# Performance work log

Measured on AMD Instinct MI355X. Metric: run time of the kernel, lower is better.

## Reference

```python
import jax, jax.numpy as jnp
import numpy as np

W = 128
POS_FREQ = 10  # -> 3*10*2 = 60 encoded dims
VIEW_FREQ = 4  # -> 3*4*2 = 24 encoded dims


def freq_encode(v, n_freq):
    # tcnn 'Frequency' encoding: sin/cos of 2^j * pi * x per input dim.
    scales = (2.0 ** jnp.arange(n_freq, dtype=v.dtype)) * jnp.pi  # [F]
    ang = v[..., :, None] * scales  # [N, 3, F]
    enc = jnp.stack([jnp.sin(ang), jnp.cos(ang)], axis=-1)  # [N, 3, F, 2]
    return enc.reshape(v.shape[0], -1)  # [N, 3*F*2]


def mlp(h, weights):
    # tcnn FullyFusedMLP: bias-free, ReLU on hidden layers, linear output.
    for Wm in weights[:-1]:
        h = jax.nn.relu(h @ Wm)
    return h @ weights[-1]


def setup_inputs():
    key = jax.random.key(0)
    ks = jax.random.split(key, 10)
    N = 1048576

    def w(k, fan_in, fan_out):
        s = (1.0 / np.sqrt(fan_in)).astype(np.float32)
        return jax.random.uniform(k, (fan_in, fan_out), jnp.float32, -s, s)

    return {
        "x": jax.random.uniform(ks[0], (N, 6), jnp.float32),
        "Wd1_0": w(ks[1], 60, W),
        "Wd1_1": w(ks[2], W, W),
        "Wd1_2": w(ks[3], W, W),
        "Wd2_0": w(ks[4], 60 + W, W),
        "Wd2_1": w(ks[5], W, W),
        "Wd2_2": w(ks[6], W, W),
        "Wd2_3": w(ks[7], W, W + 1),
        "Wc_0": w(ks[8], 24 + W, W),
        "Wc_1": w(ks[9], W, 3),
    }


def reference(x, Wd1_0, Wd1_1, Wd1_2, Wd2_0, Wd2_1, Wd2_2, Wd2_3, Wc_0, Wc_1):
    pos, view = x[:, :3], x[:, 3:6]
    # Density MLP
    enc_pos = freq_encode(pos, POS_FREQ)                # [N, 60]
    part1 = mlp(enc_pos, [Wd1_0, Wd1_1, Wd1_2])          # [N, 128]
    dens_out = mlp(jnp.concatenate([enc_pos, part1], -1),
                   [Wd2_0, Wd2_1, Wd2_2, Wd2_3])         # [N, 129]
    blending = jax.nn.sigmoid(dens_out[:, :1])           # [N, 1]
    feature = dens_out[:, 1:]                            # [N, 128]
    density = feature[:, 0:1]                            # [N, 1]
    # Color MLP
    enc_view = freq_encode(view, VIEW_FREQ)              # [N, 24]
    rgb = mlp(jnp.concatenate([enc_view, feature], -1), [Wc_0, Wc_1])  # [N, 3]
    return jnp.concatenate([rgb, density, blending], -1)  # [N, 5]
```

## Files before the change

kernel.cpp:

```cpp
#include <hip/hip_runtime.h>
#include <cstdint>
#include <cstddef>

typedef __attribute__((ext_vector_type(8))) __bf16 bf16x8;
typedef __attribute__((ext_vector_type(16))) float floatx16;

struct SrcPtrs { const float* p[9]; };


__global__ void prep_zero(unsigned short* __restrict__ ws) {
  uint4* p = (uint4*)ws;
  const int n = 143360 / 8;
  for (int i = blockIdx.x * blockDim.x + threadIdx.x; i < n; i += gridDim.x * blockDim.x)
    p[i] = make_uint4(0u, 0u, 0u, 0u);
}

__global__ void prep_fill(SrcPtrs sp, unsigned short* __restrict__ ws) {
  const int m  = blockIdx.x >> 4;
  const int sl = blockIdx.x & 15;
  const int K[9]  = {60, 128, 128, 188, 128, 128, 128, 152, 128};
  const int N[9]  = {128, 128, 128, 128, 128, 128, 129, 128, 3};
  const int SS[9] = {4, 8, 8, 12, 8, 8, 8, 10, 8};
  const unsigned OFF[9] = {0u, 8192u, 24576u, 40960u, 65536u, 81920u, 98304u, 118784u, 139264u};
  const int Km = K[m], Nm = N[m], Sm = SS[m];
  const float* __restrict__ src = sp.p[m];
  unsigned short* __restrict__ dst = ws + OFF[m];
  const int tot = Km * Nm;
  for (int i = sl * 256 + (int)threadIdx.x; i < tot; i += 16 * 256) {
    int k = i / Nm;
    int n = i - k * Nm;
    int kk = k, row = n;
    if (m == 3) kk = (k < 60) ? 128 + k : k - 60;
    if (m == 7) kk = (k < 24) ? 128 + k : k - 24;
    if (m == 6) row = (n == 0) ? 128 : n - 1;
    const int t = row >> 5, l31 = row & 31;
    const int s = kk >> 4, q2 = (kk >> 3) & 1, j = kk & 7;
    dst[(t * Sm + s) * 512 + (q2 * 32 + l31) * 8 + j] =
        __builtin_bit_cast(unsigned short, (__bf16)src[i]);
  }
}


#if defined(__has_builtin)
#if __has_builtin(__builtin_amdgcn_permlane32_swap)
#define HAVE_PLSWAP 1
#endif
#endif
#ifndef HAVE_PLSWAP
#define HAVE_PLSWAP 0
#endif

__device__ __forceinline__ unsigned pk2(float a, float b) {
  unsigned short ua = __builtin_bit_cast(unsigned short, (__bf16)a);
  unsigned short ub = __builtin_bit_cast(unsigned short, (__bf16)b);
  return (unsigned)ua | ((unsigned)ub << 16);
}

__device__ __forceinline__ void stage16(const void* g, void* l) {
  __builtin_amdgcn_global_load_lds(
      (const __attribute__((address_space(1))) unsigned int*)g,
      (__attribute__((address_space(3))) unsigned int*)l, 16, 0, 0);
}

__device__ __forceinline__ void half_swap(unsigned a, unsigned b, int q2,
                                          unsigned& lo, unsigned& hi) {
#if HAVE_PLSWAP
  auto r = __builtin_amdgcn_permlane32_swap(a, b, false, false);
  lo = r[0]; hi = r[1];
#else
  unsigned sa = __shfl_xor(a, 32, 64);
  unsigned sb = __shfl_xor(b, 32, 64);
  lo = q2 ? sb : a;
  hi = q2 ? b : sa;
#endif
}

template <int KIND>
__device__ __forceinline__ bf16x8 trig_frag(const float (&x)[6], int q2, int sl) {
  bf16x8 r;
#pragma unroll
  for (int j = 0; j < 8; ++j) {
    const int kA = 16 * sl + j;
    const int kB = 16 * sl + 8 + j;
    int dA, dB; float scA, scB; bool vA, vB;
    if (KIND == 0) {
      vA = kA < 60; vB = kB < 60;
      dA = kA / 20; dB = kB / 20;
      scA = (float)(1 << ((kA % 20) >> 1)) * 0.5f;
      scB = (float)(1 << ((kB % 20) >> 1)) * 0.5f;
    } else {
      vA = kA < 24; vB = kB < 24;
      dA = 3 + (kA >> 3); dB = 3 + (kB >> 3);
      scA = (float)(1 << ((kA & 7) >> 1)) * 0.5f;
      scB = (float)(1 << ((kB & 7) >> 1)) * 0.5f;
    }
    float v  = q2 ? x[dB] : x[dA];
    float sc = q2 ? scB : scA;
    bool ok  = q2 ? vB : vA;
    float rev = v * sc;
    float t = (j & 1) ? __builtin_amdgcn_cosf(rev) : __builtin_amdgcn_sinf(rev);
    r[j] = (__bf16)(ok ? t : 0.0f);
  }
  return r;
}

template <int S, int SL, int NT, int HT, int PP, bool RELU, int OUTM>
__device__ __forceinline__ void run_layer(const unsigned short* __restrict__ wsrc,
                                          const unsigned short* __restrict__ nsrc, int nbytes,
                                          unsigned short* __restrict__ sWt,
                                          uint2 (&pkv)[2][16],
                                          const bf16x8 (&tail)[2][4],
                                          float* __restrict__ out, int base, int tid) {
  const int lane = tid & 63;
  const int w = tid >> 6;
  const int q2 = lane >> 5;
  const int l31 = lane & 31;
  const int pt0 = base + w * 64 + l31;
  const int pt1 = pt0 + 32;

  __syncthreads();

  if (nbytes > 0) {
    const uint4* __restrict__ s4 = (const uint4*)nsrc;
    uint4* __restrict__ dst = (uint4*)(sWt + (PP ^ 1) * 12288);
    const int n16 = nbytes / 16;
    for (int i = tid; i < n16; i += 256)
      stage16(s4 + i, dst + (i & ~63));
  }

  bf16x8 bf[2][SL > 0 ? SL : 1];
#pragma unroll
  for (int s = 0; s < SL; ++s) {
#pragma unroll
    for (int m = 0; m < 2; ++m) {
      uint2 p0 = pkv[m][2 * s], p1 = pkv[m][2 * s + 1];
      unsigned w0, w1, w2, w3;
      half_swap(p0.x, p1.x, q2, w0, w2);
      half_swap(p0.y, p1.y, q2, w1, w3);
      uint4 u = make_uint4(w0, w1, w2, w3);
      bf[m][s] = __builtin_bit_cast(bf16x8, u);
    }
  }

  const unsigned short* __restrict__ ldsbuf = sWt + PP * 12288;
  const uint4* __restrict__ wp = (const uint4*)wsrc;
#pragma unroll
  for (int t = 0; t < NT; ++t) {
    floatx16 acc[2];
#pragma unroll
    for (int i = 0; i < 16; ++i) { acc[0][i] = 0.0f; acc[1][i] = 0.0f; }
#pragma unroll
    for (int s = 0; s < S; ++s) {
      bf16x8 A;
      if (t < HT) {
        A = *(const bf16x8*)&ldsbuf[(t * S + s) * 512 + lane * 8];
      } else {
        uint4 a4 = wp[(t * S + s) * 64 + lane];
        A = __builtin_bit_cast(bf16x8, a4);
      }
      bf16x8 B0 = (s < SL) ? bf[0][s < SL ? s : 0] : tail[0][s - SL];
      bf16x8 B1 = (s < SL) ? bf[1][s < SL ? s : 0] : tail[1][s - SL];
      acc[0] = __builtin_amdgcn_mfma_f32_32x32x16_bf16(A, B0, acc[0], 0, 0, 0);
      acc[1] = __builtin_amdgcn_mfma_f32_32x32x16_bf16(A, B1, acc[1], 0, 0, 0);
    }
    if (OUTM == 2) {
      if (q2 == 0) {
        float* o0 = out + (size_t)pt0 * 5;
        o0[0] = acc[0][0]; o0[1] = acc[0][1]; o0[2] = acc[0][2];
        float* o1 = out + (size_t)pt1 * 5;
        o1[0] = acc[1][0]; o1[1] = acc[1][1]; o1[2] = acc[1][2];
      }
    } else {
      if (OUTM == 0 || t < 4) {
#pragma unroll
        for (int m = 0; m < 2; ++m) {
#pragma unroll
          for (int gg = 0; gg < 4; ++gg) {
            float b0 = acc[m][4 * gg], b1 = acc[m][4 * gg + 1];
            float b2 = acc[m][4 * gg + 2], b3 = acc[m][4 * gg + 3];
            if (RELU) {
              b0 = fmaxf(b0, 0.f); b1 = fmaxf(b1, 0.f);
              b2 = fmaxf(b2, 0.f); b3 = fmaxf(b3, 0.f);
            }
            pkv[m][4 * t + gg] = make_uint2(pk2(b0, b1), pk2(b2, b3));
          }
        }
      }
      if (OUTM == 1 && q2 == 0) {
        if (t == 0) {
          out[(size_t)pt0 * 5 + 3] = acc[0][0];
          out[(size_t)pt1 * 5 + 3] = acc[1][0];
        }
        if (t == 4) {
          out[(size_t)pt0 * 5 + 4] = 1.0f / (1.0f + __expf(-acc[0][0]));
          out[(size_t)pt1 * 5 + 4] = 1.0f / (1.0f + __expf(-acc[1][0]));
        }
      }
    }
  }
}

__global__ __launch_bounds__(256, 2) void nerf_main(const float* __restrict__ x,
                                                    const unsigned short* __restrict__ ws,
                                                    float* __restrict__ out) {
  __shared__ __align__(16) unsigned short sWt[2 * 12288];

  const int tid = (int)threadIdx.x;
  const int base = (int)blockIdx.x * 256;
  const int lane = tid & 63;
  const int w = tid >> 6;
  const int q2 = lane >> 5;
  const int l31 = lane & 31;
  const int pt0 = base + w * 64 + l31;

  {
    const uint4* s4 = (const uint4*)ws;
    uint4* dst = (uint4*)sWt;
#pragma unroll
    for (int i = 0; i < 2; ++i)
      stage16(s4 + i * 256 + tid, dst + ((i * 256 + tid) & ~63));
  }

  float x0[6], x1[6];
  {
    const float* a = x + (size_t)pt0 * 6;
    const float* b = x + (size_t)(pt0 + 32) * 6;
#pragma unroll
    for (int c = 0; c < 3; ++c) {
      float2 u = *(const float2*)(a + 2 * c);
      float2 v = *(const float2*)(b + 2 * c);
      x0[2 * c] = u.x; x0[2 * c + 1] = u.y;
      x1[2 * c] = v.x; x1[2 * c + 1] = v.y;
    }
  }

  bf16x8 pkt[2][4];
#pragma unroll
  for (int sl = 0; sl < 4; ++sl) {
    pkt[0][sl] = trig_frag<0>(x0, q2, sl);
    pkt[1][sl] = trig_frag<0>(x1, q2, sl);
  }

  uint2 pkv[2][16];

  run_layer< 4, 0, 4, 2, 0, true , 0>(ws + 0u,      ws + 8192u,   16384, sWt, pkv, pkt, out, base, tid);
  run_layer< 8, 8, 4, 2, 1, true , 0>(ws + 8192u,   ws + 24576u,  16384, sWt, pkv, pkt, out, base, tid);
  run_layer< 8, 8, 4, 2, 0, false, 0>(ws + 24576u,  ws + 40960u,  24576, sWt, pkv, pkt, out, base, tid);
  run_layer<12, 8, 4, 2, 1, true , 0>(ws + 40960u,  ws + 65536u,  16384, sWt, pkv, pkt, out, base, tid);
  run_layer< 8, 8, 4, 2, 0, true , 0>(ws + 65536u,  ws + 81920u,  16384, sWt, pkv, pkt, out, base, tid);
  run_layer< 8, 8, 4, 2, 1, true , 0>(ws + 81920u,  ws + 98304u,  24576, sWt, pkv, pkt, out, base, tid);
  run_layer< 8, 8, 5, 3, 0, false, 1>(ws + 98304u,  ws + 118784u, 20480, sWt, pkv, pkt, out, base, tid);

  bf16x8 vw[2][4];
#pragma unroll
  for (int sl = 0; sl < 2; ++sl) {
    vw[0][sl] = trig_frag<1>(x0, q2, sl);
    vw[1][sl] = trig_frag<1>(x1, q2, sl);
  }
  vw[0][2] = vw[0][0]; vw[0][3] = vw[0][0];
  vw[1][2] = vw[1][0]; vw[1][3] = vw[1][0];

  run_layer<10, 8, 4, 2, 1, true , 0>(ws + 118784u, ws + 139264u,  8192, sWt, pkv, vw,  out, base, tid);
  run_layer< 8, 8, 1, 1, 0, false, 2>(ws + 139264u, (const unsigned short*)nullptr, 0, sWt, pkv, pkt, out, base, tid);
}

extern "C" void kernel_launch(void* const* d_in, const int* in_sizes, int n_in,
                              void* d_out, int out_size, void* d_ws, size_t ws_size,
                              hipStream_t stream) {
  (void)n_in; (void)out_size; (void)ws_size;
  const float* x = (const float*)d_in[0];
  SrcPtrs sp;
  for (int i = 0; i < 9; ++i) sp.p[i] = (const float*)d_in[1 + i];
  unsigned short* ws = (unsigned short*)d_ws;
  float* out = (float*)d_out;
  const int N = in_sizes[0] / 6;

  prep_zero<<<70, 256, 0, stream>>>(ws);
  prep_fill<<<144, 256, 0, stream>>>(sp, ws);
  nerf_main<<<N / 256, 256, 0, stream>>>(x, ws, out);
}
```

Before: 360.6 us.

## Process one 32-point tile per wave with 512-thread blocks and on-the-fly trig

Each wave now handles 32 points instead of 64, so blocks grow to 512 threads (8 waves) with launch bounds targeting 4 blocks per CU. Activations are kept directly as bf16 MFMA fragments with the half-swap done at the layer output, and the positional encoding is recomputed per layer rather than held in registers. More of each weight matrix is staged into shared memory (HF fragments), fewer are read from global. The aim is lower register pressure and higher occupancy, at the cost of redundant sin/cos work and half as many points sharing each weight fragment load.

```diff
diff --git a/kernel.cpp b/kernel.cpp
--- a/kernel.cpp
+++ b/kernel.cpp
@@ -104,19 +104,18 @@
   return r;
 }
 
-template <int S, int SL, int NT, int HT, int PP, bool RELU, int OUTM>
+template <int S, int SL, int ST, int KIND, int NT, int HF, int PP, bool RELU, int OUTM>
 __device__ __forceinline__ void run_layer(const unsigned short* __restrict__ wsrc,
                                           const unsigned short* __restrict__ nsrc, int nbytes,
                                           unsigned short* __restrict__ sWt,
-                                          uint2 (&pkv)[2][16],
-                                          const bf16x8 (&tail)[2][4],
+                                          const bf16x8 (&bfin)[8], bf16x8 (&bfout)[8],
+                                          const float (&x)[6],
                                           float* __restrict__ out, int base, int tid) {
   const int lane = tid & 63;
   const int w = tid >> 6;
   const int q2 = lane >> 5;
   const int l31 = lane & 31;
-  const int pt0 = base + w * 64 + l31;
-  const int pt1 = pt0 + 32;
+  const int pt = base + w * 32 + l31;
 
   __syncthreads();
 
@@ -124,83 +123,72 @@
     const uint4* __restrict__ s4 = (const uint4*)nsrc;
     uint4* __restrict__ dst = (uint4*)(sWt + (PP ^ 1) * 12288);
     const int n16 = nbytes / 16;
-    for (int i = tid; i < n16; i += 256)
+    for (int i = tid; i < n16; i += 512)
       stage16(s4 + i, dst + (i & ~63));
   }
 
-  bf16x8 bf[2][SL > 0 ? SL : 1];
-#pragma unroll
-  for (int s = 0; s < SL; ++s) {
-#pragma unroll
-    for (int m = 0; m < 2; ++m) {
-      uint2 p0 = pkv[m][2 * s], p1 = pkv[m][2 * s + 1];
-      unsigned w0, w1, w2, w3;
-      half_swap(p0.x, p1.x, q2, w0, w2);
-      half_swap(p0.y, p1.y, q2, w1, w3);
-      uint4 u = make_uint4(w0, w1, w2, w3);
-      bf[m][s] = __builtin_bit_cast(bf16x8, u);
-    }
-  }
+  bf16x8 tail[ST > 0 ? ST : 1];
+#pragma unroll
+  for (int j = 0; j < ST; ++j) tail[j] = trig_frag<KIND>(x, q2, j);
 
   const unsigned short* __restrict__ ldsbuf = sWt + PP * 12288;
   const uint4* __restrict__ wp = (const uint4*)wsrc;
 #pragma unroll
   for (int t = 0; t < NT; ++t) {
-    floatx16 acc[2];
-#pragma unroll
-    for (int i = 0; i < 16; ++i) { acc[0][i] = 0.0f; acc[1][i] = 0.0f; }
+    floatx16 acc;
+#pragma unroll
+    for (int i = 0; i < 16; ++i) acc[i] = 0.0f;
 #pragma unroll
     for (int s = 0; s < S; ++s) {
+      constexpr int dummy = 0; (void)dummy;
+      const int f = t * S + s;
       bf16x8 A;
-      if (t < HT) {
-        A = *(const bf16x8*)&ldsbuf[(t * S + s) * 512 + lane * 8];
+      if (f < HF) {
+        A = *(const bf16x8*)&ldsbuf[f * 512 + lane * 8];
       } else {
-        uint4 a4 = wp[(t * S + s) * 64 + lane];
+        uint4 a4 = wp[f * 64 + lane];
         A = __builtin_bit_cast(bf16x8, a4);
       }
-      bf16x8 B0 = (s < SL) ? bf[0][s < SL ? s : 0] : tail[0][s - SL];
-      bf16x8 B1 = (s < SL) ? bf[1][s < SL ? s : 0] : tail[1][s - SL];
-      acc[0] = __builtin_amdgcn_mfma_f32_32x32x16_bf16(A, B0, acc[0], 0, 0, 0);
-      acc[1] = __builtin_amdgcn_mfma_f32_32x32x16_bf16(A, B1, acc[1], 0, 0, 0);
+      bf16x8 B = (s < SL) ? bfin[(s < SL) ? s : 0] : tail[s - SL];
+      acc = __builtin_amdgcn_mfma_f32_32x32x16_bf16(A, B, acc, 0, 0, 0);
     }
     if (OUTM == 2) {
       if (q2 == 0) {
-        float* o0 = out + (size_t)pt0 * 5;
-        o0[0] = acc[0][0]; o0[1] = acc[0][1]; o0[2] = acc[0][2];
-        float* o1 = out + (size_t)pt1 * 5;
-        o1[0] = acc[1][0]; o1[1] = acc[1][1]; o1[2] = acc[1][2];
+        float* o = out + (size_t)pt * 5;
+        o[0] = acc[0]; o[1] = acc[1]; o[2] = acc[2];
       }
     } else {
       if (OUTM == 0 || t < 4) {
 #pragma unroll
-        for (int m = 0; m < 2; ++m) {
-#pragma unroll
-          for (int gg = 0; gg < 4; ++gg) {
-            float b0 = acc[m][4 * gg], b1 = acc[m][4 * gg + 1];
-            float b2 = acc[m][4 * gg + 2], b3 = acc[m][4 * gg + 3];
-            if (RELU) {
-              b0 = fmaxf(b0, 0.f); b1 = fmaxf(b1, 0.f);
-              b2 = fmaxf(b2, 0.f); b3 = fmaxf(b3, 0.f);
-            }
-            pkv[m][4 * t + gg] = make_uint2(pk2(b0, b1), pk2(b2, b3));
+        for (int h = 0; h < 2; ++h) {
+          float a0 = acc[8 * h + 0], a1 = acc[8 * h + 1];
+          float a2 = acc[8 * h + 2], a3 = acc[8 * h + 3];
+          float b0 = acc[8 * h + 4], b1 = acc[8 * h + 5];
+          float b2 = acc[8 * h + 6], b3 = acc[8 * h + 7];
+          if (RELU) {
+            a0 = fmaxf(a0, 0.f); a1 = fmaxf(a1, 0.f);
+            a2 = fmaxf(a2, 0.f); a3 = fmaxf(a3, 0.f);
+            b0 = fmaxf(b0, 0.f); b1 = fmaxf(b1, 0.f);
+            b2 = fmaxf(b2, 0.f); b3 = fmaxf(b3, 0.f);
           }
+          unsigned p0x = pk2(a0, a1), p0y = pk2(a2, a3);
+          unsigned p1x = pk2(b0, b1), p1y = pk2(b2, b3);
+          unsigned w0, w1, w2, w3;
+          half_swap(p0x, p1x, q2, w0, w2);
+          half_swap(p0y, p1y, q2, w1, w3);
+          bfout[2 * t + h] = __builtin_bit_cast(bf16x8, make_uint4(w0, w1, w2, w3));
         }
       }
       if (OUTM == 1 && q2 == 0) {
-        if (t == 0) {
-          out[(size_t)pt0 * 5 + 3] = acc[0][0];
-          out[(size_t)pt1 * 5 + 3] = acc[1][0];
-        }
-        if (t == 4) {
-          out[(size_t)pt0 * 5 + 4] = 1.0f / (1.0f + __expf(-acc[0][0]));
-          out[(size_t)pt1 * 5 + 4] = 1.0f / (1.0f + __expf(-acc[1][0]));
-        }
-      }
-    }
-  }
-}
-
-__global__ __launch_bounds__(256, 2) void nerf_main(const float* __restrict__ x,
+        if (t == 0) out[(size_t)pt * 5 + 3] = acc[0];
+        if (t == 4)
+          out[(size_t)pt * 5 + 4] = 1.0f / (1.0f + __expf(-acc[0]));
+      }
+    }
+  }
+}
+
+__global__ __launch_bounds__(512, 4) void nerf_main(const float* __restrict__ x,
                                                     const unsigned short* __restrict__ ws,
                                                     float* __restrict__ out) {
   __shared__ __align__(16) unsigned short sWt[2 * 12288];
@@ -211,57 +199,37 @@
   const int w = tid >> 6;
   const int q2 = lane >> 5;
   const int l31 = lane & 31;
-  const int pt0 = base + w * 64 + l31;
+  const int pt = base + w * 32 + l31;
 
   {
     const uint4* s4 = (const uint4*)ws;
     uint4* dst = (uint4*)sWt;
 #pragma unroll
     for (int i = 0; i < 2; ++i)
-      stage16(s4 + i * 256 + tid, dst + ((i * 256 + tid) & ~63));
-  }
-
-  float x0[6], x1[6];
+      stage16(s4 + i * 512 + tid, dst + ((i * 512 + tid) & ~63));
+  }
+
+  float x6[6];
   {
-    const float* a = x + (size_t)pt0 * 6;
-    const float* b = x + (size_t)(pt0 + 32) * 6;
+    const float* a = x + (size_t)pt * 6;
 #pragma unroll
     for (int c = 0; c < 3; ++c) {
       float2 u = *(const float2*)(a + 2 * c);
-      float2 v = *(const float2*)(b + 2 * c);
-      x0[2 * c] = u.x; x0[2 * c + 1] = u.y;
-      x1[2 * c] = v.x; x1[2 * c + 1] = v.y;
-    }
-  }
-
-  bf16x8 pkt[2][4];
-#pragma unroll
-  for (int sl = 0; sl < 4; ++sl) {
-    pkt[0][sl] = trig_frag<0>(x0, q2, sl);
-    pkt[1][sl] = trig_frag<0>(x1, q2, sl);
-  }
-
-  uint2 pkv[2][16];
-
-  run_layer< 4, 0, 4, 2, 0, true , 0>(ws + 0u,      ws + 8192u,   16384, sWt, pkv, pkt, out, base, tid);
-  run_layer< 8, 8, 4, 2, 1, true , 0>(ws + 8192u,   ws + 24576u,  16384, sWt, pkv, pkt, out, base, tid);
-  run_layer< 8, 8, 4, 2, 0, false, 0>(ws + 24576u,  ws + 40960u,  24576, sWt, pkv, pkt, out, base, tid);
-  run_layer<12, 8, 4, 2, 1, true , 0>(ws + 40960u,  ws + 65536u,  16384, sWt, pkv, pkt, out, base, tid);
-  run_layer< 8, 8, 4, 2, 0, true , 0>(ws + 65536u,  ws + 81920u,  16384, sWt, pkv, pkt, out, base, tid);
-  run_layer< 8, 8, 4, 2, 1, true , 0>(ws + 81920u,  ws + 98304u,  24576, sWt, pkv, pkt, out, base, tid);
-  run_layer< 8, 8, 5, 3, 0, false, 1>(ws + 98304u,  ws + 118784u, 20480, sWt, pkv, pkt, out, base, tid);
-
-  bf16x8 vw[2][4];
-#pragma unroll
-  for (int sl = 0; sl < 2; ++sl) {
-    vw[0][sl] = trig_frag<1>(x0, q2, sl);
-    vw[1][sl] = trig_frag<1>(x1, q2, sl);
-  }
-  vw[0][2] = vw[0][0]; vw[0][3] = vw[0][0];
-  vw[1][2] = vw[1][0]; vw[1][3] = vw[1][0];
-
-  run_layer<10, 8, 4, 2, 1, true , 0>(ws + 118784u, ws + 139264u,  8192, sWt, pkv, vw,  out, base, tid);
-  run_layer< 8, 8, 1, 1, 0, false, 2>(ws + 139264u, (const unsigned short*)nullptr, 0, sWt, pkv, pkt, out, base, tid);
+      x6[2 * c] = u.x; x6[2 * c + 1] = u.y;
+    }
+  }
+
+  bf16x8 F1[8], F2[8];
+
+  run_layer< 4, 0, 4, 0, 4, 16, 0, true , 0>(ws + 0u,      ws + 8192u,   24576, sWt, F2, F1, x6, out, base, tid);
+  run_layer< 8, 8, 0, 0, 4, 24, 1, true , 0>(ws + 8192u,   ws + 24576u,  24576, sWt, F1, F2, x6, out, base, tid);
+  run_layer< 8, 8, 0, 0, 4, 24, 0, false, 0>(ws + 24576u,  ws + 40960u,  24576, sWt, F2, F1, x6, out, base, tid);
+  run_layer<12, 8, 4, 0, 4, 24, 1, true , 0>(ws + 40960u,  ws + 65536u,  24576, sWt, F1, F2, x6, out, base, tid);
+  run_layer< 8, 8, 0, 0, 4, 24, 0, true , 0>(ws + 65536u,  ws + 81920u,  24576, sWt, F2, F1, x6, out, base, tid);
+  run_layer< 8, 8, 0, 0, 4, 24, 1, true , 0>(ws + 81920u,  ws + 98304u,  24576, sWt, F1, F2, x6, out, base, tid);
+  run_layer< 8, 8, 0, 0, 5, 24, 0, false, 1>(ws + 98304u,  ws + 118784u, 24576, sWt, F2, F1, x6, out, base, tid);
+  run_layer<10, 8, 2, 1, 4, 24, 1, true , 0>(ws + 118784u, ws + 139264u,  8192, sWt, F1, F2, x6, out, base, tid);
+  run_layer< 8, 8, 0, 0, 1,  8, 0, false, 2>(ws + 139264u, (const unsigned short*)nullptr, 0, sWt, F2, F1, x6, out, base, tid);
 }
 
 extern "C" void kernel_launch(void* const* d_in, const int* in_sizes, int n_in,
@@ -277,5 +245,5 @@
 
   prep_zero<<<70, 256, 0, stream>>>(ws);
   prep_fill<<<144, 256, 0, stream>>>(sp, ws);
-  nerf_main<<<N / 256, 256, 0, stream>>>(x, ws, out);
-}
+  nerf_main<<<N / 256, 512, 0, stream>>>(x, ws, out);
+}
```

New measurement: 383.7 us. +6.4%, slower.
